# Kernel tuning notes

Hardware: AMD Instinct MI355X
Metric: run time of the kernel (lower is better)

The kernel has to match this reference:

```python
import jax, jax.numpy as jnp
import numpy as np

D_MODEL, D_INNER, D_STATE, D_CONV, DT_RANK = 4, 8, 16, 4, 1


def _build_perms(N, H, W):
    # center-out 2D spatial order
    yy, xx = np.meshgrid(np.arange(H), np.arange(W), indexing='ij')
    cy, cx = H // 2, W // 2
    d2 = (yy - cy) ** 2 + (xx - cx) ** 2
    sp = np.argsort(d2.reshape(-1), kind='stable')          # (H*W,)
    HW = H * W
    # scanA: for each frame t, full center-out spatial sweep
    scanA = (np.arange(N)[:, None] * HW + sp[None, :]).reshape(-1)
    # scanB: for each spatial pos (in center-out order), zig-zag over frames
    fwd = np.arange(N)
    bwd = fwd[::-1]
    tids = np.where((np.arange(HW) % 2 == 0)[:, None], fwd[None, :], bwd[None, :])  # (HW, N)
    scanB = (tids * HW + sp[:, None]).reshape(-1)
    perms = np.stack([scanA, scanB, scanA[::-1], scanB[::-1]], axis=0)  # (4, L)
    return jnp.asarray(perms)


def _dwconv1d(x_bcl, w, b, pad, groups):
    # x: (B, C, L), w: (C, 1, K) depthwise
    y = jax.lax.conv_general_dilated(x_bcl, w, (1,), [pad],
                                     feature_group_count=groups,
                                     dimension_numbers=('NCH', 'OIH', 'NCH'))
    return y + b[None, :, None]


def _forward(x, dwconv_w, dwconv_b, in_proj_w, conv1d_w, conv1d_b,
             x_proj_w, dt_proj_w, dt_proj_b, A_log, Dp, out_proj_w, ln_g, ln_b):
    B, N, H, W = x.shape
    L = N * H * W
    perms = _build_perms(N, H, W)                 # (4, L) int, static
    xf = x.reshape(B, L)
    seqs = xf[:, perms]                            # (B, 4, L) gather along 4 scans
    seqs = _dwconv1d(seqs, dwconv_w, dwconv_b, (1, 1), 4)
    u = jax.nn.silu(seqs.transpose(0, 2, 1))       # (B, L, 4)
    # ---- Mamba(d_model=4) ----
    xz = jnp.einsum('bld,ed->ble', u, in_proj_w)   # (B, L, 2*d_inner)
    xm, z = xz[..., :D_INNER], xz[..., D_INNER:]
    xc = _dwconv1d(xm.transpose(0, 2, 1), conv1d_w, conv1d_b, (D_CONV - 1, 0), D_INNER)
    xm = jax.nn.silu(xc.transpose(0, 2, 1))        # (B, L, 8) causal conv + SiLU
    x_dbl = jnp.einsum('bld,ed->ble', xm, x_proj_w)  # (B, L, dt_rank+2*d_state)
    dt = x_dbl[..., :DT_RANK]
    Bm = x_dbl[..., DT_RANK:DT_RANK + D_STATE]     # (B, L, 16)
    Cm = x_dbl[..., DT_RANK + D_STATE:]            # (B, L, 16)
    dt = jax.nn.softplus(jnp.einsum('blr,dr->bld', dt, dt_proj_w) + dt_proj_b)  # (B, L, 8)
    A = -jnp.exp(A_log)                            # (8, 16)
    dA = jnp.exp(dt[..., None] * A)                # (B, L, 8, 16)
    dBx = dt[..., None] * Bm[:, :, None, :] * xm[..., None]  # (B, L, 8, 16)

    def step(h, inp):
        dA_t, dBx_t, C_t = inp
        h = dA_t * h + dBx_t                       # (B, 8, 16)
        return h, jnp.einsum('bds,bs->bd', h, C_t)

    h0 = jnp.zeros((B, D_INNER, D_STATE), x.dtype)
    _, ys = jax.lax.scan(step, h0, (dA.transpose(1, 0, 2, 3),
                                    dBx.transpose(1, 0, 2, 3),
                                    Cm.transpose(1, 0, 2)))
    y = ys.transpose(1, 0, 2) + xm * Dp            # (B, L, 8)
    y = y * jax.nn.silu(z)
    out = jnp.einsum('bld,ed->ble', y, out_proj_w)  # (B, L, 4)
    # ---- LayerNorm(4) ----
    mu = out.mean(-1, keepdims=True)
    var = ((out - mu) ** 2).mean(-1, keepdims=True)
    out = (out - mu) * jax.lax.rsqrt(var + 1e-5) * ln_g + ln_b
    # rec[:, inv[i]] = out[:, :, i]  <=>  rec_i = out[:, perms[i], i]
    rec = jnp.take_along_axis(out, perms.T[None], axis=1)  # (B, L, 4)
    return rec.mean(-1).reshape(B, N, H, W)


def setup_inputs() -> dict:
    key = jax.random.key(0)
    ks = jax.random.split(key, 12)
    s = 0.1
    x = jax.random.normal(ks[0], (4, 6, 128, 128), jnp.float32)
    return {
        'x': x,
        'dwconv_w': jax.random.normal(ks[1], (4, 1, 3), jnp.float32) * s,
        'dwconv_b': jnp.zeros((4,), jnp.float32),
        'in_proj_w': jax.random.normal(ks[2], (2 * D_INNER, D_MODEL), jnp.float32) * s,
        'conv1d_w': jax.random.normal(ks[3], (D_INNER, 1, D_CONV), jnp.float32) * s,
        'conv1d_b': jnp.zeros((D_INNER,), jnp.float32),
        'x_proj_w': jax.random.normal(ks[4], (DT_RANK + 2 * D_STATE, D_INNER), jnp.float32) * s,
        'dt_proj_w': jax.random.normal(ks[5], (D_INNER, DT_RANK), jnp.float32) * s,
        'dt_proj_b': jnp.full((D_INNER,), -2.0, jnp.float32),
        'A_log': jnp.log(jnp.tile(jnp.arange(1, D_STATE + 1, dtype=jnp.float32), (D_INNER, 1))),
        'Dp': jnp.ones((D_INNER,), jnp.float32),
        'out_proj_w': jax.random.normal(ks[6], (D_MODEL, D_INNER), jnp.float32) * s,
        'ln_g': jnp.ones((4,), jnp.float32),
        'ln_b': jnp.zeros((4,), jnp.float32),
    }


def reference(x, dwconv_w, dwconv_b, in_proj_w, conv1d_w, conv1d_b,
              x_proj_w, dt_proj_w, dt_proj_b, A_log, Dp, out_proj_w, ln_g, ln_b):
    return _forward(x, dwconv_w, dwconv_b, in_proj_w, conv1d_w, conv1d_b,
                    x_proj_w, dt_proj_w, dt_proj_b, A_log, Dp, out_proj_w, ln_g, ln_b)
```

## Files before the change

### kernel.cpp

```cpp
#include <hip/hip_runtime.h>
#include <math.h>

#define HWSZ  16384
#define LTOT  98304
#define NB    4
#define TCH   96
#define NCH   1024
#define SD    100
#define NBL   (NB * LTOT)

__device__ __forceinline__ float siluf(float x){
  return x * __builtin_amdgcn_rcpf(1.f + __expf(-x));
}
__device__ __forceinline__ float softplusf(float x){
  return fmaxf(x, 0.f) + __logf(1.f + __expf(-fabsf(x)));
}

__device__ __forceinline__ float red16(float x){
  int v;
  v = __float_as_int(x);
  x += __int_as_float(__builtin_amdgcn_update_dpp(0, v, 0xB1, 0xF, 0xF, true));
  v = __float_as_int(x);
  x += __int_as_float(__builtin_amdgcn_update_dpp(0, v, 0x4E, 0xF, 0xF, true));
  v = __float_as_int(x);
  x += __int_as_float(__builtin_amdgcn_update_dpp(0, v, 0x141, 0xF, 0xF, true));
  v = __float_as_int(x);
  x += __int_as_float(__builtin_amdgcn_update_dpp(0, v, 0x140, 0xF, 0xF, true));
  return x;
}

__device__ __forceinline__ int isqrt_floor(int v){
  int r = __float2int_rn(sqrtf((float)v));
  if (r * r > v) --r;
  else if ((r + 1) * (r + 1) <= v) ++r;
  return r;
}

__device__ __forceinline__ int rho0(int i, const int* __restrict__ sp){
  int n = i >> 14; int r = i & (HWSZ - 1);
  return (n << 14) + sp[r];
}
__device__ __forceinline__ int rho1(int i, const int* __restrict__ sp){
  unsigned ui = (unsigned)i;
  unsigned r = ui / 6u; unsigned n = ui - r * 6u;
  unsigned t = (r & 1u) ? (5u - n) : n;
  return (int)((t << 14) + (unsigned)sp[r]);
}

__global__ __launch_bounds__(128) void k_rank(int* __restrict__ sp){
  const int j = blockIdx.x * 128 + threadIdx.x;
  const int y = j >> 7, x = j & 127;
  const int dy = y - 64, dx = x - 64;
  const int v = dy*dy + dx*dx;
  int cnt = 0;
  for (int yy = 0; yy < 128; ++yy){
    int dyy = yy - 64;
    int w = v - dyy*dyy;
    if (w > 0){
      int m = isqrt_floor(w - 1);
      int lo = m < 64 ? m : 64;
      int hi = m < 63 ? m : 63;
      cnt += lo + hi + 1;
    }
  }
  {
    const int r = isqrt_floor(v);
    int yp0 = 64 - r; if (yp0 < 0) yp0 = 0;
    int yp1 = 64 + r + 1; if (yp1 > y) yp1 = y;
    for (int yp = yp0; yp < yp1; ++yp){
      int dyp = yp - 64;
      int tt = v - dyp*dyp;
      int rr = isqrt_floor(tt);
      if (rr * rr == tt){
        cnt += (rr <= 64) ? 1 : 0;
        cnt += (rr >= 1 && rr <= 63) ? 1 : 0;
      }
    }
    if (x > 64) cnt += 1;
  }
  sp[cnt] = j;
}

__global__ __launch_bounds__(128, 4)
void k_scan(const float* __restrict__ X,
            const float* __restrict__ dww, const float* __restrict__ dwb,
            const float* __restrict__ ipw,
            const float* __restrict__ c1w, const float* __restrict__ c1b,
            const float* __restrict__ xpw,
            const float* __restrict__ dtpw, const float* __restrict__ dtpb,
            const float* __restrict__ Alog,
            const int* __restrict__ sp,
            float* __restrict__ chA, float* __restrict__ chB,
            float* __restrict__ y0g,
            float* __restrict__ Cg,  float* __restrict__ xmg,
            float* __restrict__ zsg, float* __restrict__ sgg)
{
  const int c = blockIdx.x, b = blockIdx.y;
  const int c0 = c * TCH;
  const int tid = threadIdx.x;
  const float* Xb = X + (size_t)b * LTOT;
  const size_t cb = (size_t)b * NCH + c;

  __shared__ __align__(16) float s_pre[(TCH + 3) * 9];
  __shared__ __align__(16) float s_dt[8 * SD];
  __shared__ __align__(16) float s_dxm[8 * SD];
  __shared__ __align__(16) float s_Bv[16 * SD];
  __shared__ __align__(16) float s_Cv[16 * SD];

  if (tid < TCH + 3){
    const int m = tid;
    const int i = c0 - 3 + m;
    if (i < 0){
      #pragma unroll
      for (int d = 0; d < 8; ++d) s_pre[m*9 + d] = 0.f;
    } else {
      const int i2 = LTOT - 1 - i;
      const bool okm = (i > 0), okp = (i < LTOT - 1);
      int q[12];
      q[0]  = okm ? rho0(i - 1, sp) : 0;
      q[1]  =       rho0(i,     sp);
      q[2]  = okp ? rho0(i + 1, sp) : 0;
      q[3]  = okm ? rho1(i - 1, sp) : 0;
      q[4]  =       rho1(i,     sp);
      q[5]  = okp ? rho1(i + 1, sp) : 0;
      q[6]  = okm ? rho0(i2 + 1, sp) : 0;
      q[7]  =       rho0(i2,     sp);
      q[8]  = okp ? rho0(i2 - 1, sp) : 0;
      q[9]  = okm ? rho1(i2 + 1, sp) : 0;
      q[10] =       rho1(i2,     sp);
      q[11] = okp ? rho1(i2 - 1, sp) : 0;
      float xv[12];
      #pragma unroll
      for (int t = 0; t < 12; ++t) xv[t] = Xb[q[t]];
      if (!okm){ xv[0] = 0.f; xv[3] = 0.f; xv[6] = 0.f; xv[9]  = 0.f; }
      if (!okp){ xv[2] = 0.f; xv[5] = 0.f; xv[8] = 0.f; xv[11] = 0.f; }
      float u[4];
      #pragma unroll
      for (int k = 0; k < 4; ++k){
        float acc = dwb[k];
        acc = fmaf(dww[k*3+0], xv[k*3+0], acc);
        acc = fmaf(dww[k*3+1], xv[k*3+1], acc);
        acc = fmaf(dww[k*3+2], xv[k*3+2], acc);
        u[k] = siluf(acc);
      }
      #pragma unroll
      for (int d = 0; d < 8; ++d){
        float acc =      ipw[d*4+0] * u[0];
        acc = fmaf(ipw[d*4+1], u[1], acc);
        acc = fmaf(ipw[d*4+2], u[2], acc);
        acc = fmaf(ipw[d*4+3], u[3], acc);
        s_pre[m*9 + d] = acc;
      }
      if (m >= 3){
        const int t0 = m - 3;
        float zs8[8];
        #pragma unroll
        for (int d = 0; d < 8; ++d){
          float acc =      ipw[(8+d)*4+0] * u[0];
          acc = fmaf(ipw[(8+d)*4+1], u[1], acc);
          acc = fmaf(ipw[(8+d)*4+2], u[2], acc);
          acc = fmaf(ipw[(8+d)*4+3], u[3], acc);
          zs8[d] = siluf(acc);
        }
        float* pz = zsg + (cb*96 + t0)*8;
        *reinterpret_cast<float4*>(pz)     = make_float4(zs8[0], zs8[1], zs8[2], zs8[3]);
        *reinterpret_cast<float4*>(pz + 4) = make_float4(zs8[4], zs8[5], zs8[6], zs8[7]);
      }
    }
  }
  __syncthreads();

  if (tid < TCH){
    const int t = tid;
    float xm[8];
    #pragma unroll
    for (int d = 0; d < 8; ++d){
      float acc = c1b[d];
      #pragma unroll
      for (int tau = 0; tau < 4; ++tau)
        acc = fmaf(c1w[d*4+tau], s_pre[(t+tau)*9 + d], acc);
      xm[d] = siluf(acc);
    }
    {
      float* px = xmg + (cb*96 + t)*8;
      *reinterpret_cast<float4*>(px)     = make_float4(xm[0], xm[1], xm[2], xm[3]);
      *reinterpret_cast<float4*>(px + 4) = make_float4(xm[4], xm[5], xm[6], xm[7]);
    }
    float dtr = xpw[0] * xm[0];
    #pragma unroll
    for (int d = 1; d < 8; ++d) dtr = fmaf(xpw[d], xm[d], dtr);
    float C16[16];
    #pragma unroll
    for (int s = 0; s < 16; ++s){
      float acc = xpw[(1+s)*8] * xm[0];
      #pragma unroll
      for (int d = 1; d < 8; ++d) acc = fmaf(xpw[(1+s)*8+d], xm[d], acc);
      s_Bv[s*SD + t] = acc;
      float acc2 = xpw[(17+s)*8] * xm[0];
      #pragma unroll
      for (int d = 1; d < 8; ++d) acc2 = fmaf(xpw[(17+s)*8+d], xm[d], acc2);
      s_Cv[s*SD + t] = acc2;
      C16[s] = acc2;
    }
    {
      float* pc = Cg + (cb*96 + t)*16;
      #pragma unroll
      for (int s4 = 0; s4 < 16; s4 += 4)
        *reinterpret_cast<float4*>(pc + s4) = make_float4(C16[s4], C16[s4+1], C16[s4+2], C16[s4+3]);
    }
    #pragma unroll
    for (int d = 0; d < 8; ++d){
      float dtv = softplusf(fmaf(dtpw[d], dtr, dtpb[d]));
      s_dt[d*SD + t]  = dtv;
      s_dxm[d*SD + t] = dtv * xm[d];
    }
  }
  __syncthreads();

  {
    const int d = tid >> 4, s = tid & 15;
    const float Ads = -__expf(Alog[tid]);
    float h = 0.f, sdt = 0.f;
    const float* pdt = s_dt + d*SD;
    const float* pdx = s_dxm + d*SD;
    const float* pB  = s_Bv + s*SD;
    const float* pC  = s_Cv + s*SD;
    float* yb = y0g + cb * 768 + d * 96;
    float* sb = sgg + (cb*8 + d) * 96;
    for (int t0 = 0; t0 < TCH; t0 += 4){
      const float4 dt4 = *reinterpret_cast<const float4*>(pdt + t0);
      const float4 dx4 = *reinterpret_cast<const float4*>(pdx + t0);
      const float4 B4  = *reinterpret_cast<const float4*>(pB + t0);
      const float4 C4  = *reinterpret_cast<const float4*>(pC + t0);
      float r0 = sdt + dt4.x, r1 = r0 + dt4.y, r2 = r1 + dt4.z, r3 = r2 + dt4.w;
      sdt = r3;
      float y0, y1, y2, y3;
      { float dA = __expf(dt4.x*Ads); h = fmaf(dA, h, dx4.x*B4.x); y0 = h*C4.x; }
      { float dA = __expf(dt4.y*Ads); h = fmaf(dA, h, dx4.y*B4.y); y1 = h*C4.y; }
      { float dA = __expf(dt4.z*Ads); h = fmaf(dA, h, dx4.z*B4.z); y2 = h*C4.z; }
      { float dA = __expf(dt4.w*Ads); h = fmaf(dA, h, dx4.w*B4.w); y3 = h*C4.w; }
      y0 = red16(y0); y1 = red16(y1); y2 = red16(y2); y3 = red16(y3);
      if (s == 0){
        *reinterpret_cast<float4*>(yb + t0) = make_float4(y0, y1, y2, y3);
        *reinterpret_cast<float4*>(sb + t0) = make_float4(r0, r1, r2, r3);
      }
    }
    const size_t base = cb * 128 + tid;
    chA[base] = __expf(Ads * sdt);
    chB[base] = h;
  }
}

__global__ __launch_bounds__(128) void k_comb(const float* __restrict__ chA,
                                              const float* __restrict__ chB,
                                              float* __restrict__ hin){
  const int wave = (blockIdx.x << 1) | (threadIdx.x >> 6);
  const int lane = threadIdx.x & 63;
  const int b   = wave >> 7;
  const int idx = wave & 127;
  const size_t basebi = (size_t)b * NCH * 128 + idx;
  float carry = 0.f;
  float a = chA[basebi + (size_t)lane * 128];
  float h = chB[basebi + (size_t)lane * 128];
  for (int seg = 0; seg < NCH / 64; ++seg){
    float aN = 1.f, hN = 0.f;
    if (seg + 1 < NCH / 64){
      const size_t off = basebi + (size_t)((seg + 1) * 64 + lane) * 128;
      aN = chA[off]; hN = chB[off];
    }
    #pragma unroll
    for (int o = 1; o < 64; o <<= 1){
      float aj = __shfl_up(a, o, 64);
      float hj = __shfl_up(h, o, 64);
      if (lane >= o){ h = fmaf(a, hj, h); a *= aj; }
    }
    float ae = __shfl_up(a, 1, 64);
    float he = __shfl_up(h, 1, 64);
    if (lane == 0){ ae = 1.f; he = 0.f; }
    hin[basebi + (size_t)(seg * 64 + lane) * 128] = fmaf(ae, carry, he);
    float aL = __shfl(a, 63, 64);
    float hL = __shfl(h, 63, 64);
    carry = fmaf(aL, carry, hL);
    a = aN; h = hN;
  }
}

__global__ __launch_bounds__(128)
void k_corr(const float* __restrict__ Cg,  const float* __restrict__ sgg,
            const float* __restrict__ xmg, const float* __restrict__ zsg,
            const float* __restrict__ Alog, const float* __restrict__ Dp,
            const float* __restrict__ opw,
            const float* __restrict__ lng, const float* __restrict__ lnb,
            const float* __restrict__ hin,
            const float* __restrict__ y0g,
            float* __restrict__ outbuf)
{
  const int c = blockIdx.x, b = blockIdx.y;
  const int c0 = c * TCH;
  const int tid = threadIdx.x;
  const size_t cb = (size_t)b * NCH + c;

  __shared__ float s_hA[256];
  __shared__ float s_yf[8 * 96];

  s_hA[tid]       = hin[cb * 128 + tid];
  s_hA[128 + tid] = -__expf(Alog[tid]);

  {
    const int d = tid >> 4, tsub = tid & 15;
    float w[16], A16[16];
    #pragma unroll
    for (int s = 0; s < 16; ++s){
      w[s]   = s_hA[d*16 + s];
      A16[s] = s_hA[128 + d*16 + s];
    }
    const float* psg = sgg + (cb*8 + d) * 96;
    const float* py0 = y0g + cb * 768 + d * 96;
    const float* pC  = Cg + cb * 96 * 16;
    #pragma unroll
    for (int t = tsub; t < TCH; t += 16){
      const float sg = psg[t];
      float acc = py0[t];
      const float* pc = pC + t*16;
      #pragma unroll
      for (int s4 = 0; s4 < 16; s4 += 4){
        const float4 C4 = *reinterpret_cast<const float4*>(pc + s4);
        acc = fmaf(C4.x, __expf(A16[s4+0]*sg) * w[s4+0], acc);
        acc = fmaf(C4.y, __expf(A16[s4+1]*sg) * w[s4+1], acc);
        acc = fmaf(C4.z, __expf(A16[s4+2]*sg) * w[s4+2], acc);
        acc = fmaf(C4.w, __expf(A16[s4+3]*sg) * w[s4+3], acc);
      }
      s_yf[d*96 + t] = acc;
    }
  }
  __syncthreads();

  if (tid < TCH){
    const int t = tid;
    const int i = c0 + t;
    const float* px = xmg + (cb*96 + t)*8;
    const float* pz = zsg + (cb*96 + t)*8;
    const float4 xa = *reinterpret_cast<const float4*>(px);
    const float4 xbv = *reinterpret_cast<const float4*>(px + 4);
    const float4 za = *reinterpret_cast<const float4*>(pz);
    const float4 zb = *reinterpret_cast<const float4*>(pz + 4);
    const float xm8[8] = {xa.x, xa.y, xa.z, xa.w, xbv.x, xbv.y, xbv.z, xbv.w};
    const float zs8[8] = {za.x, za.y, za.z, za.w, zb.x, zb.y, zb.z, zb.w};
    float y[8];
    #pragma unroll
    for (int d = 0; d < 8; ++d)
      y[d] = (s_yf[d*96 + t] + xm8[d] * Dp[d]) * zs8[d];
    float o[4];
    #pragma unroll
    for (int e = 0; e < 4; ++e){
      float acc = opw[e*8] * y[0];
      #pragma unroll
      for (int d = 1; d < 8; ++d) acc = fmaf(opw[e*8+d], y[d], acc);
      o[e] = acc;
    }
    const float mu = 0.25f * (o[0] + o[1] + o[2] + o[3]);
    const float v0 = o[0] - mu, v1 = o[1] - mu, v2 = o[2] - mu, v3 = o[3] - mu;
    const float inv = rsqrtf(0.25f * (v0*v0 + v1*v1 + v2*v2 + v3*v3) + 1e-5f);
    const size_t base = (size_t)b * LTOT + i;
    outbuf[0*NBL + base] = fmaf(v0 * inv, lng[0], lnb[0]);
    outbuf[1*NBL + base] = fmaf(v1 * inv, lng[1], lnb[1]);
    outbuf[2*NBL + base] = fmaf(v2 * inv, lng[2], lnb[2]);
    outbuf[3*NBL + base] = fmaf(v3 * inv, lng[3], lnb[3]);
  }
}

__global__ __launch_bounds__(256) void k_final(const float* __restrict__ outbuf,
                                               const int* __restrict__ sp,
                                               float* __restrict__ out){
  const int l = blockIdx.x * 256 + threadIdx.x;
  const int b = blockIdx.y;
  const int q0 = rho0(l, sp), q1 = rho1(l, sp);
  const int j  = LTOT - 1 - l;
  const int q2 = rho0(j, sp), q3 = rho1(j, sp);
  const size_t pb = (size_t)b * LTOT;
  out[pb + l] = 0.25f * (outbuf[0*NBL + pb + q0] + outbuf[1*NBL + pb + q1] +
                         outbuf[2*NBL + pb + q2] + outbuf[3*NBL + pb + q3]);
}

extern "C" void kernel_launch(void* const* d_in, const int* in_sizes, int n_in,
                              void* d_out, int out_size, void* d_ws, size_t ws_size,
                              hipStream_t stream) {
  const float* X    = (const float*)d_in[0];
  const float* dww  = (const float*)d_in[1];
  const float* dwb  = (const float*)d_in[2];
  const float* ipw  = (const float*)d_in[3];
  const float* c1w  = (const float*)d_in[4];
  const float* c1b  = (const float*)d_in[5];
  const float* xpw  = (const float*)d_in[6];
  const float* dtpw = (const float*)d_in[7];
  const float* dtpb = (const float*)d_in[8];
  const float* Alog = (const float*)d_in[9];
  const float* Dp   = (const float*)d_in[10];
  const float* opw  = (const float*)d_in[11];
  const float* lng  = (const float*)d_in[12];
  const float* lnb  = (const float*)d_in[13];
  float* out = (float*)d_out;

  int* wsI    = (int*)d_ws;
  int* sp     = wsI;
  float* chA  = (float*)(wsI + 16384);
  float* chB  = chA + 524288;
  float* hin  = chB + 524288;
  float* y0g  = hin + 524288;
  float* Cg   = y0g + 3145728;
  float* xmg  = Cg  + 6291456;
  float* zsg  = xmg + 3145728;
  float* sgg  = zsg + 3145728;
  float* outbuf = sgg + 3145728;

  k_rank<<<128, 128, 0, stream>>>(sp);
  k_scan<<<dim3(NCH, NB), 128, 0, stream>>>(X, dww, dwb, ipw, c1w, c1b, xpw,
      dtpw, dtpb, Alog, sp, chA, chB, y0g, Cg, xmg, zsg, sgg);
  k_comb<<<256, 128, 0, stream>>>(chA, chB, hin);
  k_corr<<<dim3(NCH, NB), 128, 0, stream>>>(Cg, sgg, xmg, zsg,
      Alog, Dp, opw, lng, lnb, hin, y0g, outbuf);
  k_final<<<dim3(LTOT / 256, NB), 256, 0, stream>>>(outbuf, sp, out);
}
```

Baseline: 192.4 us.

## Pre-permute input, recompute C in corr, scatter output with atomics

```diff
diff --git a/kernel.cpp b/kernel.cpp
--- a/kernel.cpp
+++ b/kernel.cpp
@@ -36,19 +36,17 @@
   return r;
 }
 
-__device__ __forceinline__ int rho0(int i, const int* __restrict__ sp){
-  int n = i >> 14; int r = i & (HWSZ - 1);
-  return (n << 14) + sp[r];
-}
-__device__ __forceinline__ int rho1(int i, const int* __restrict__ sp){
-  unsigned ui = (unsigned)i;
-  unsigned r = ui / 6u; unsigned n = ui - r * 6u;
-  unsigned t = (r & 1u) ? (5u - n) : n;
-  return (int)((t << 14) + (unsigned)sp[r]);
-}
-
-__global__ __launch_bounds__(128) void k_rank(int* __restrict__ sp){
+__global__ __launch_bounds__(128) void k_prep(const float* __restrict__ X,
+                                              int* __restrict__ spinv,
+                                              float* __restrict__ xs0,
+                                              float* __restrict__ xs1,
+                                              float* __restrict__ out){
   const int j = blockIdx.x * 128 + threadIdx.x;
+  {
+    float4* o4 = (float4*)out;
+    const float4 z4 = make_float4(0.f, 0.f, 0.f, 0.f);
+    for (int k = j; k < NBL / 4; k += HWSZ) o4[k] = z4;
+  }
   const int y = j >> 7, x = j & 127;
   const int dy = y - 64, dx = x - 64;
   const int v = dy*dy + dx*dx;
@@ -78,27 +76,38 @@
     }
     if (x > 64) cnt += 1;
   }
-  sp[cnt] = j;
+  spinv[j] = cnt;
+  #pragma unroll
+  for (int b = 0; b < NB; ++b){
+    const float* Xb = X + (size_t)b * LTOT;
+    float* p0 = xs0 + (size_t)b * LTOT;
+    float* p1 = xs1 + (size_t)b * LTOT;
+    #pragma unroll
+    for (int m = 0; m < 6; ++m){
+      const float xv = Xb[m * HWSZ + j];
+      p0[m * HWSZ + cnt] = xv;
+      const int n1 = (cnt & 1) ? (5 - m) : m;
+      p1[cnt * 6 + n1] = xv;
+    }
+  }
 }
 
 __global__ __launch_bounds__(128, 4)
-void k_scan(const float* __restrict__ X,
+void k_scan(const float* __restrict__ xs0, const float* __restrict__ xs1,
             const float* __restrict__ dww, const float* __restrict__ dwb,
             const float* __restrict__ ipw,
             const float* __restrict__ c1w, const float* __restrict__ c1b,
             const float* __restrict__ xpw,
             const float* __restrict__ dtpw, const float* __restrict__ dtpb,
             const float* __restrict__ Alog,
-            const int* __restrict__ sp,
             float* __restrict__ chA, float* __restrict__ chB,
             float* __restrict__ y0g,
-            float* __restrict__ Cg,  float* __restrict__ xmg,
-            float* __restrict__ zsg, float* __restrict__ sgg)
+            float* __restrict__ xmg, float* __restrict__ zsg,
+            float* __restrict__ sgg)
 {
   const int c = blockIdx.x, b = blockIdx.y;
   const int c0 = c * TCH;
   const int tid = threadIdx.x;
-  const float* Xb = X + (size_t)b * LTOT;
   const size_t cb = (size_t)b * NCH + c;
 
   __shared__ __align__(16) float s_pre[(TCH + 3) * 9];
@@ -114,26 +123,23 @@
       #pragma unroll
       for (int d = 0; d < 8; ++d) s_pre[m*9 + d] = 0.f;
     } else {
-      const int i2 = LTOT - 1 - i;
+      const float* p0 = xs0 + (size_t)b * LTOT;
+      const float* p1 = xs1 + (size_t)b * LTOT;
+      const int iL = LTOT - 1 - i;
       const bool okm = (i > 0), okp = (i < LTOT - 1);
-      int q[12];
-      q[0]  = okm ? rho0(i - 1, sp) : 0;
-      q[1]  =       rho0(i,     sp);
-      q[2]  = okp ? rho0(i + 1, sp) : 0;
-      q[3]  = okm ? rho1(i - 1, sp) : 0;
-      q[4]  =       rho1(i,     sp);
-      q[5]  = okp ? rho1(i + 1, sp) : 0;
-      q[6]  = okm ? rho0(i2 + 1, sp) : 0;
-      q[7]  =       rho0(i2,     sp);
-      q[8]  = okp ? rho0(i2 - 1, sp) : 0;
-      q[9]  = okm ? rho1(i2 + 1, sp) : 0;
-      q[10] =       rho1(i2,     sp);
-      q[11] = okp ? rho1(i2 - 1, sp) : 0;
       float xv[12];
-      #pragma unroll
-      for (int t = 0; t < 12; ++t) xv[t] = Xb[q[t]];
-      if (!okm){ xv[0] = 0.f; xv[3] = 0.f; xv[6] = 0.f; xv[9]  = 0.f; }
-      if (!okp){ xv[2] = 0.f; xv[5] = 0.f; xv[8] = 0.f; xv[11] = 0.f; }
+      xv[0]  = okm ? p0[i - 1]  : 0.f;
+      xv[1]  =       p0[i];
+      xv[2]  = okp ? p0[i + 1]  : 0.f;
+      xv[3]  = okm ? p1[i - 1]  : 0.f;
+      xv[4]  =       p1[i];
+      xv[5]  = okp ? p1[i + 1]  : 0.f;
+      xv[6]  = okm ? p0[iL + 1] : 0.f;
+      xv[7]  =       p0[iL];
+      xv[8]  = okp ? p0[iL - 1] : 0.f;
+      xv[9]  = okm ? p1[iL + 1] : 0.f;
+      xv[10] =       p1[iL];
+      xv[11] = okp ? p1[iL - 1] : 0.f;
       float u[4];
       #pragma unroll
       for (int k = 0; k < 4; ++k){
@@ -189,7 +195,6 @@
     float dtr = xpw[0] * xm[0];
     #pragma unroll
     for (int d = 1; d < 8; ++d) dtr = fmaf(xpw[d], xm[d], dtr);
-    float C16[16];
     #pragma unroll
     for (int s = 0; s < 16; ++s){
       float acc = xpw[(1+s)*8] * xm[0];
@@ -200,13 +205,6 @@
       #pragma unroll
       for (int d = 1; d < 8; ++d) acc2 = fmaf(xpw[(17+s)*8+d], xm[d], acc2);
       s_Cv[s*SD + t] = acc2;
-      C16[s] = acc2;
-    }
-    {
-      float* pc = Cg + (cb*96 + t)*16;
-      #pragma unroll
-      for (int s4 = 0; s4 < 16; s4 += 4)
-        *reinterpret_cast<float4*>(pc + s4) = make_float4(C16[s4], C16[s4+1], C16[s4+2], C16[s4+3]);
     }
     #pragma unroll
     for (int d = 0; d < 8; ++d){
@@ -286,14 +284,15 @@
 }
 
 __global__ __launch_bounds__(128)
-void k_corr(const float* __restrict__ Cg,  const float* __restrict__ sgg,
-            const float* __restrict__ xmg, const float* __restrict__ zsg,
+void k_corr(const float* __restrict__ xmg, const float* __restrict__ zsg,
+            const float* __restrict__ sgg, const float* __restrict__ y0g,
+            const float* __restrict__ hin,
+            const float* __restrict__ xpw,
             const float* __restrict__ Alog, const float* __restrict__ Dp,
             const float* __restrict__ opw,
             const float* __restrict__ lng, const float* __restrict__ lnb,
-            const float* __restrict__ hin,
-            const float* __restrict__ y0g,
-            float* __restrict__ outbuf)
+            const int* __restrict__ spinv,
+            float* __restrict__ out)
 {
   const int c = blockIdx.x, b = blockIdx.y;
   const int c0 = c * TCH;
@@ -301,10 +300,27 @@
   const size_t cb = (size_t)b * NCH + c;
 
   __shared__ float s_hA[256];
+  __shared__ __align__(16) float s_Ct[96 * 20];
   __shared__ float s_yf[8 * 96];
 
   s_hA[tid]       = hin[cb * 128 + tid];
   s_hA[128 + tid] = -__expf(Alog[tid]);
+
+  if (tid < TCH){
+    const float* px = xmg + (cb*96 + tid)*8;
+    const float4 xa = *reinterpret_cast<const float4*>(px);
+    const float4 xb = *reinterpret_cast<const float4*>(px + 4);
+    const float xm8[8] = {xa.x, xa.y, xa.z, xa.w, xb.x, xb.y, xb.z, xb.w};
+    float* pct = s_Ct + tid*20;
+    #pragma unroll
+    for (int s = 0; s < 16; ++s){
+      float acc = xpw[(17+s)*8] * xm8[0];
+      #pragma unroll
+      for (int d = 1; d < 8; ++d) acc = fmaf(xpw[(17+s)*8+d], xm8[d], acc);
+      pct[s] = acc;
+    }
+  }
+  __syncthreads();
 
   {
     const int d = tid >> 4, tsub = tid & 15;
@@ -316,12 +332,11 @@
     }
     const float* psg = sgg + (cb*8 + d) * 96;
     const float* py0 = y0g + cb * 768 + d * 96;
-    const float* pC  = Cg + cb * 96 * 16;
     #pragma unroll
     for (int t = tsub; t < TCH; t += 16){
       const float sg = psg[t];
       float acc = py0[t];
-      const float* pc = pC + t*16;
+      const float* pc = s_Ct + t*20;
       #pragma unroll
       for (int s4 = 0; s4 < 16; s4 += 4){
         const float4 C4 = *reinterpret_cast<const float4*>(pc + s4);
@@ -341,10 +356,10 @@
     const float* px = xmg + (cb*96 + t)*8;
     const float* pz = zsg + (cb*96 + t)*8;
     const float4 xa = *reinterpret_cast<const float4*>(px);
-    const float4 xbv = *reinterpret_cast<const float4*>(px + 4);
+    const float4 xb = *reinterpret_cast<const float4*>(px + 4);
     const float4 za = *reinterpret_cast<const float4*>(pz);
     const float4 zb = *reinterpret_cast<const float4*>(pz + 4);
-    const float xm8[8] = {xa.x, xa.y, xa.z, xa.w, xbv.x, xbv.y, xbv.z, xbv.w};
+    const float xm8[8] = {xa.x, xa.y, xa.z, xa.w, xb.x, xb.y, xb.z, xb.w};
     const float zs8[8] = {za.x, za.y, za.z, za.w, zb.x, zb.y, zb.z, zb.w};
     float y[8];
     #pragma unroll
@@ -361,25 +376,21 @@
     const float mu = 0.25f * (o[0] + o[1] + o[2] + o[3]);
     const float v0 = o[0] - mu, v1 = o[1] - mu, v2 = o[2] - mu, v3 = o[3] - mu;
     const float inv = rsqrtf(0.25f * (v0*v0 + v1*v1 + v2*v2 + v3*v3) + 1e-5f);
-    const size_t base = (size_t)b * LTOT + i;
-    outbuf[0*NBL + base] = fmaf(v0 * inv, lng[0], lnb[0]);
-    outbuf[1*NBL + base] = fmaf(v1 * inv, lng[1], lnb[1]);
-    outbuf[2*NBL + base] = fmaf(v2 * inv, lng[2], lnb[2]);
-    outbuf[3*NBL + base] = fmaf(v3 * inv, lng[3], lnb[3]);
-  }
-}
-
-__global__ __launch_bounds__(256) void k_final(const float* __restrict__ outbuf,
-                                               const int* __restrict__ sp,
-                                               float* __restrict__ out){
-  const int l = blockIdx.x * 256 + threadIdx.x;
-  const int b = blockIdx.y;
-  const int q0 = rho0(l, sp), q1 = rho1(l, sp);
-  const int j  = LTOT - 1 - l;
-  const int q2 = rho0(j, sp), q3 = rho1(j, sp);
-  const size_t pb = (size_t)b * LTOT;
-  out[pb + l] = 0.25f * (outbuf[0*NBL + pb + q0] + outbuf[1*NBL + pb + q1] +
-                         outbuf[2*NBL + pb + q2] + outbuf[3*NBL + pb + q3]);
+    const float w0 = fmaf(v0 * inv, lng[0], lnb[0]);
+    const float w1 = fmaf(v1 * inv, lng[1], lnb[1]);
+    const float w2 = fmaf(v2 * inv, lng[2], lnb[2]);
+    const float w3 = fmaf(v3 * inv, lng[3], lnb[3]);
+    const int n = i >> 14, j = i & (HWSZ - 1);
+    const int r = spinv[j];
+    const int l0 = (n << 14) + r;
+    const int n1 = (r & 1) ? (5 - n) : n;
+    const int l1 = r * 6 + n1;
+    float* ob = out + (size_t)b * LTOT;
+    atomicAdd(ob + l0,            0.25f * w0);
+    atomicAdd(ob + l1,            0.25f * w1);
+    atomicAdd(ob + (LTOT-1 - l0), 0.25f * w2);
+    atomicAdd(ob + (LTOT-1 - l1), 0.25f * w3);
+  }
 }
 
 extern "C" void kernel_launch(void* const* d_in, const int* in_sizes, int n_in,
@@ -401,23 +412,22 @@
   const float* lnb  = (const float*)d_in[13];
   float* out = (float*)d_out;
 
-  int* wsI    = (int*)d_ws;
-  int* sp     = wsI;
-  float* chA  = (float*)(wsI + 16384);
-  float* chB  = chA + 524288;
-  float* hin  = chB + 524288;
-  float* y0g  = hin + 524288;
-  float* Cg   = y0g + 3145728;
-  float* xmg  = Cg  + 6291456;
-  float* zsg  = xmg + 3145728;
-  float* sgg  = zsg + 3145728;
-  float* outbuf = sgg + 3145728;
-
-  k_rank<<<128, 128, 0, stream>>>(sp);
-  k_scan<<<dim3(NCH, NB), 128, 0, stream>>>(X, dww, dwb, ipw, c1w, c1b, xpw,
-      dtpw, dtpb, Alog, sp, chA, chB, y0g, Cg, xmg, zsg, sgg);
+  int* wsI     = (int*)d_ws;
+  int* spinv   = wsI;
+  float* xs0   = (float*)(wsI + 16384);
+  float* xs1   = xs0 + NBL;
+  float* chA   = xs1 + NBL;
+  float* chB   = chA + 524288;
+  float* hin   = chB + 524288;
+  float* y0g   = hin + 524288;
+  float* xmg   = y0g + 3145728;
+  float* zsg   = xmg + 3145728;
+  float* sgg   = zsg + 3145728;
+
+  k_prep<<<128, 128, 0, stream>>>(X, spinv, xs0, xs1, out);
+  k_scan<<<dim3(NCH, NB), 128, 0, stream>>>(xs0, xs1, dww, dwb, ipw, c1w, c1b, xpw,
+      dtpw, dtpb, Alog, chA, chB, y0g, xmg, zsg, sgg);
   k_comb<<<256, 128, 0, stream>>>(chA, chB, hin);
-  k_corr<<<dim3(NCH, NB), 128, 0, stream>>>(Cg, sgg, xmg, zsg,
-      Alog, Dp, opw, lng, lnb, hin, y0g, outbuf);
-  k_final<<<dim3(LTOT / 256, NB), 256, 0, stream>>>(outbuf, sp, out);
-}
+  k_corr<<<dim3(NCH, NB), 128, 0, stream>>>(xmg, zsg, sgg, y0g, hin,
+      xpw, Alog, Dp, opw, lng, lnb, spinv, out);
+}
```

Result: slower. 247.1 us (+28.4%).
